# Kernel optimization log

Measured on AMD Instinct MI355X. Metric: run time of the kernel, lower is better.

## Reference

```python
import jax, jax.numpy as jnp
import numpy as np

# Deterministic stand-ins for the torch RNG draws in the original forward
# (rot sampled from {0,40,...,320}, shifts from [-20,20], flips from {2,3}).
ROT_DEG = 40.0          # rotations[1]
SHIFTS = (5, -7)        # roll shifts on (H, W)
FLIP_DIMS = (2, 3)      # flip W and D dims (torch.arange(2,4) both selected)


def _rotate_nn_maps(H, W, deg):
    """Nearest-neighbor inverse-rotation index maps for an HxW grid
    (matches torchvision rotate: nearest interp, expand=False, fill=0)."""
    theta = jnp.deg2rad(jnp.float32(deg))
    cy = (H - 1) / 2.0
    cx = (W - 1) / 2.0
    i = jnp.arange(H, dtype=jnp.float32)[:, None] - cy  # [H,1]
    j = jnp.arange(W, dtype=jnp.float32)[None, :] - cx  # [1,W]
    c, s = jnp.cos(theta), jnp.sin(theta)
    # inverse rotation: map each output pixel back to its source location
    src_i = c * i + s * j + cy
    src_j = -s * i + c * j + cx
    si = jnp.round(src_i).astype(jnp.int32)
    sj = jnp.round(src_j).astype(jnp.int32)
    valid = (si >= 0) & (si < H) & (sj >= 0) & (sj < W)
    return jnp.clip(si, 0, H - 1), jnp.clip(sj, 0, W - 1), valid


def setup_inputs() -> dict:
    key = jax.random.key(0)
    features = jax.random.normal(key, (16, 128, 128, 8, 16), dtype=jnp.float32)
    return {"features": features}


def reference(features):
    # features: [B, H, W, D, F]; one fused gather rotates the (H, W) plane for
    # every (sample, depth, feature) simultaneously, replacing the original
    # per-(sample, feature) Python rotate() loop.
    B, H, W, D, F = features.shape
    si, sj, valid = _rotate_nn_maps(H, W, ROT_DEG)
    rotated = jnp.where(valid[None, :, :, None, None],
                        features[:, si, sj, :, :], 0.0)  # [B,H,W,D,F]
    rolled = jnp.roll(rotated, SHIFTS, axis=(1, 2))
    flipped = jnp.flip(rolled, axis=FLIP_DIMS)
    return flipped
```

## Files before the change

kernel.cpp:

```cpp
#include <hip/hip_runtime.h>
#include <math.h>


typedef float f32x4 __attribute__((ext_vector_type(4)));

#define HH 128
#define WW 128

__global__ __launch_bounds__(1024) void aug_tiled(const f32x4* __restrict__ in,
                                                  f32x4* __restrict__ out) {
    int blk = blockIdx.x;
    int tw0 = (blk & 3) << 5;
    int th0 = ((blk >> 2) & 3) << 5;
    int b   = blk >> 4;

    int t  = threadIdx.x;
    int f4 = t & 3;
    int d  = (t >> 2) & 7;
    int wp = t >> 5;
    int dd = 7 - d;

    int w = tw0 + wp;
    int j = (134 - w) & 127;

    const double c = 0.76604444311897803;
    const double s = 0.64278760968653933;
    double dj = (double)j - 63.5;
    double sjc = c * dj + 63.5;
    double sic = s * dj + 63.5;

    long long base_b = (long long)b * (HH * WW * 8 * 4);

    #pragma unroll 4
    for (int hp = 0; hp < 32; ++hp) {
        int h = th0 + hp;
        int i = (h + 123) & 127;
        double di = (double)i - 63.5;
        int si = (int)rint(c * di + sic);
        int sj = (int)rint(-s * di + sjc);
        bool valid = (si >= 0) & (si < HH) & (sj >= 0) & (sj < WW);

        f32x4 v = (f32x4)(0.f);
        if (valid) {
            long long src = base_b + (long long)(((si * WW + sj) * 8 + dd) * 4 + f4);
            v = in[src];
        }
        long long dst = base_b + (long long)(((h * WW + w) * 8 + d) * 4 + f4);
        __builtin_nontemporal_store(v, &out[dst]);
    }
}

extern "C" void kernel_launch(void* const* d_in, const int* in_sizes, int n_in,
                              void* d_out, int out_size, void* d_ws, size_t ws_size,
                              hipStream_t stream) {
    const f32x4* in = (const f32x4*)d_in[0];
    f32x4* out = (f32x4*)d_out;
    aug_tiled<<<256, 1024, 0, stream>>>(in, out);
}
```

Measured before the change: 230.5 us.

## Replace gather rotation with coalesced-read scatter plus separate zero-fill kernel

The per-output gather loop becomes a scatter. Each thread reads one input vector with a fully coalesced load, forward-rotates its source pixel, tests a 2x2 neighbourhood of output pixels whose nearest-neighbour inverse maps back to that source, and writes to each match. A second small kernel zero-fills output pixels whose inverse source falls outside the image. The launch goes from 256 large blocks with a serial loop to many small blocks, trading an extra kernel launch and some fp64 math for more parallelism and contiguous reads. The 2x2 candidate window may miss outputs near the rounding boundary, which risks correctness.

```diff
diff --git a/kernel.cpp b/kernel.cpp
--- a/kernel.cpp
+++ b/kernel.cpp
@@ -7,47 +7,74 @@
 #define HH 128
 #define WW 128
 
-__global__ __launch_bounds__(1024) void aug_tiled(const f32x4* __restrict__ in,
-                                                  f32x4* __restrict__ out) {
-    int blk = blockIdx.x;
-    int tw0 = (blk & 3) << 5;
-    int th0 = ((blk >> 2) & 3) << 5;
-    int b   = blk >> 4;
+__global__ __launch_bounds__(256) void aug_scatter(const f32x4* __restrict__ in,
+                                                   f32x4* __restrict__ out) {
+    int tid = blockIdx.x * 256 + threadIdx.x;
+    f32x4 v = in[tid];
 
-    int t  = threadIdx.x;
-    int f4 = t & 3;
-    int d  = (t >> 2) & 7;
-    int wp = t >> 5;
-    int dd = 7 - d;
-
-    int w = tw0 + wp;
-    int j = (134 - w) & 127;
+    int q    = tid & 31;
+    int f4   = q & 3;
+    int dd   = q >> 2;
+    int sblk = tid >> 5;
+    int sj = sblk & 127;
+    int si = (sblk >> 7) & 127;
+    int b  = sblk >> 14;
 
     const double c = 0.76604444311897803;
     const double s = 0.64278760968653933;
-    double dj = (double)j - 63.5;
-    double sjc = c * dj + 63.5;
-    double sic = s * dj + 63.5;
+    double dsi = (double)si - 63.5;
+    double dsj = (double)sj - 63.5;
+    double fi = c * dsi - s * dsj + 63.5;
+    double fj = s * dsi + c * dsj + 63.5;
+    int i0 = (int)floor(fi);
+    int j0 = (int)floor(fj);
 
+    int d_out = 7 - dd;
     long long base_b = (long long)b * (HH * WW * 8 * 4);
 
-    #pragma unroll 4
-    for (int hp = 0; hp < 32; ++hp) {
-        int h = th0 + hp;
-        int i = (h + 123) & 127;
+    #pragma unroll
+    for (int ci = 0; ci < 2; ++ci) {
+        int i = i0 + ci;
+        if ((unsigned)i >= 128u) continue;
         double di = (double)i - 63.5;
-        int si = (int)rint(c * di + sic);
-        int sj = (int)rint(-s * di + sjc);
-        bool valid = (si >= 0) & (si < HH) & (sj >= 0) & (sj < WW);
+        #pragma unroll
+        for (int cj = 0; cj < 2; ++cj) {
+            int j = j0 + cj;
+            if ((unsigned)j >= 128u) continue;
+            double dj = (double)j - 63.5;
+            int ri = (int)rint(c * di + s * dj + 63.5);
+            int rj = (int)rint(-s * di + c * dj + 63.5);
+            if (ri == si && rj == sj) {
+                int h = (i + 5) & 127;
+                int w = (134 - j) & 127;
+                long long dst = base_b + (long long)(((h * WW + w) * 8 + d_out) * 4 + f4);
+                out[dst] = v;
+            }
+        }
+    }
+}
 
-        f32x4 v = (f32x4)(0.f);
-        if (valid) {
-            long long src = base_b + (long long)(((si * WW + sj) * 8 + dd) * 4 + f4);
-            v = in[src];
-        }
-        long long dst = base_b + (long long)(((h * WW + w) * 8 + d) * 4 + f4);
-        __builtin_nontemporal_store(v, &out[dst]);
-    }
+__global__ __launch_bounds__(256) void aug_zero_invalid(f32x4* __restrict__ out) {
+    int t = blockIdx.x * 256 + threadIdx.x;
+    int half = t & 1;
+    int b = (t >> 1) & 15;
+    int w = (t >> 5) & 127;
+    int h = t >> 12;
+
+    int i = (h + 123) & 127;
+    int j = (134 - w) & 127;
+    const double c = 0.76604444311897803;
+    const double s = 0.64278760968653933;
+    double di = (double)i - 63.5;
+    double dj = (double)j - 63.5;
+    int si = (int)rint(c * di + s * dj + 63.5);
+    int sj = (int)rint(-s * di + c * dj + 63.5);
+    if ((unsigned)si < 128u && (unsigned)sj < 128u) return;
+
+    long long base = ((long long)((b * 128 + h) * 128 + w)) * 32 + half * 16;
+    f32x4 z = (f32x4)(0.f);
+    #pragma unroll
+    for (int k = 0; k < 16; ++k) out[base + k] = z;
 }
 
 extern "C" void kernel_launch(void* const* d_in, const int* in_sizes, int n_in,
@@ -55,5 +82,6 @@
                               hipStream_t stream) {
     const f32x4* in = (const f32x4*)d_in[0];
     f32x4* out = (f32x4*)d_out;
-    aug_tiled<<<256, 1024, 0, stream>>>(in, out);
+    aug_scatter<<<32768, 256, 0, stream>>>(in, out);
+    aug_zero_invalid<<<2048, 256, 0, stream>>>(out);
 }
```

After: 238.9 us. 1.04x slower.
